# Performance work log

Measured on AMD Instinct MI355X. Metric: run time of the kernel, lower is better.

The kernel has to match this reference:

```python
import jax, jax.numpy as jnp
import numpy as np

B, T, I, H, A = 32, 1024, 64, 512, 16


def setup_inputs() -> dict:
    key = jax.random.key(0)
    ks = jax.random.split(key, 8)
    # xavier-normal-ish scales (faithful to init distribution family, values are arbitrary for a numeric baseline)
    def xavier(k, shape):
        fan_in, fan_out = shape[0], shape[1]
        std = (2.0 / (fan_in + fan_out)) ** 0.5
        return jax.random.normal(k, shape, dtype=jnp.float32) * std
    inp = jax.random.normal(ks[0], (B, T, I), dtype=jnp.float32)
    hn = jax.random.normal(ks[1], (1, B, H), dtype=jnp.float32)
    w_hh = xavier(ks[2], (H, H))          # weight_l0_hh: [hid, hid]
    w_ih = xavier(ks[3], (I, H))          # weight_l0_ih: [inp, hid]
    # torch Linear(hid, hid): y = x @ W.T + b; store already-transposed [in, out]
    fc1_w = xavier(ks[4], (H, H))
    fc1_b = jax.random.normal(ks[5], (H,), dtype=jnp.float32) * 0.01
    fc2_w = xavier(ks[6], (H, A))
    fc2_b = jax.random.normal(ks[7], (A,), dtype=jnp.float32) * 0.01
    return {"inp": inp, "hn": hn, "w_hh": w_hh, "w_ih": w_ih,
            "fc1_w": fc1_w, "fc1_b": fc1_b, "fc2_w": fc2_w, "fc2_b": fc2_b}


def reference(inp, hn, w_hh, w_ih, fc1_w, fc1_b, fc2_w, fc2_b):
    h0 = hn[0]                                  # [B, H]  (hn.squeeze(0))
    # precompute input projection for all steps: [T, B, H]
    x_proj = jnp.einsum('bti,ih->tbh', inp, w_ih)
    def step(h, xp_t):
        h_next = jax.nn.sigmoid(h @ w_hh + xp_t)  # [B, H]
        return h_next, h_next
    _, hs = jax.lax.scan(step, h0, x_proj)       # hs: [T, B, H]
    rnn_out = jnp.swapaxes(hs, 0, 1)             # [B, T, H]
    hn_last = rnn_out[:, -1, :][None]            # [1, B, H]
    hidden = jax.nn.relu(rnn_out @ fc1_w + fc1_b)
    out = jax.nn.sigmoid(hidden @ fc2_w + fc2_b) # [B, T, A]
    return (out, hn_last, rnn_out)
```

## Files before the change

### kernel.cpp

```cpp
#include <hip/hip_runtime.h>
#include <hip/hip_bf16.h>

#define Bz 32
#define Tz 1024
#define Iz 64
#define Hz 512
#define Az 16
#define NB 16

#define OFF_HN  (Bz*Tz*Az)
#define OFF_RNN (OFF_HN + Bz*Hz)

typedef unsigned short u16;
typedef unsigned int u32;
typedef unsigned long long u64;
typedef __attribute__((ext_vector_type(8))) unsigned short u16x8;
typedef __attribute__((ext_vector_type(8))) __bf16 bf16x8;
typedef __attribute__((ext_vector_type(4))) float f32x4;
typedef __attribute__((ext_vector_type(2))) float f32x2;

#define WS_FLAGS 0x00000u
#define WS_RING  0x21000u
#define WS_WHH   0x41000u
#define WS_WIH   0xC1000u
#define WS_W1T   0xD1000u
#define WS_ZERO  0x11000u

__device__ __forceinline__ u16 f2bf(float f) {
  union { float f; unsigned int i; } x; x.f = f;
  unsigned int r = (x.i + 0x7FFFu + ((x.i >> 16) & 1u)) >> 16;
  return (u16)r;
}
__device__ __forceinline__ float bf2f(u16 u) {
  union { unsigned int i; float f; } x; x.i = ((unsigned int)u) << 16; return x.f;
}
__device__ __forceinline__ float sigmoidf_(float z) {
  return 1.0f / (1.0f + __expf(-z));
}

__global__ void prep_kernel(const float* __restrict__ whh,
                            const float* __restrict__ wih,
                            const float* __restrict__ w1,
                            u16* __restrict__ whh_bf,
                            u16* __restrict__ wih_bf,
                            u16* __restrict__ w1t_bf) {
  int idx = blockIdx.x * 256 + threadIdx.x;
  if (idx < 262144) {
    whh_bf[idx] = f2bf(whh[idx]);
  } else if (idx < 294912) {
    int i = idx - 262144;
    wih_bf[i] = f2bf(wih[i]);
  } else if (idx < 557056) {
    int j = idx - 294912;
    int n = j >> 9, k = j & 511;
    w1t_bf[n * Hz + k] = f2bf(w1[k * Hz + n]);
  }
}

__global__ __launch_bounds__(512, 1) void rnn_scan_kernel(
    const float* __restrict__ inp,
    const float* __restrict__ hn,
    const u16* __restrict__ whh_bf,
    const u16* __restrict__ wih_bf,
    float* __restrict__ out_rnn,
    float* __restrict__ out_hn,
    int* __restrict__ flags,
    u16* __restrict__ hbuf)
{
  __shared__ float part[8 * 32 * 33];

  const int tid  = threadIdx.x;
  const int lane = tid & 63;
  const int w    = tid >> 6;
  const int ln   = lane & 15;
  const int q    = lane >> 4;
  const int c0   = blockIdx.x * 32;
  const int k0   = w * 64;

  bf16x8 bhh[2][2];
#pragma unroll
  for (int ct = 0; ct < 2; ++ct)
#pragma unroll
    for (int kc = 0; kc < 2; ++kc) {
      u16x8 f;
#pragma unroll
      for (int j = 0; j < 8; ++j)
        f[j] = whh_bf[(k0 + kc * 32 + q * 8 + j) * Hz + c0 + ct * 16 + ln];
      bhh[ct][kc] = __builtin_bit_cast(bf16x8, f);
    }

  bf16x8 bih[2];
  if (w < 2) {
#pragma unroll
    for (int ct = 0; ct < 2; ++ct) {
      u16x8 f;
#pragma unroll
      for (int j = 0; j < 8; ++j)
        f[j] = wih_bf[(w * 32 + q * 8 + j) * Hz + c0 + ct * 16 + ln];
      bih[ct] = __builtin_bit_cast(bf16x8, f);
    }
  }

  const int orow = tid >> 4;
  const int ocp  = tid & 15;
  const int ocol = c0 + ocp * 2;

  {
    u32 pk = (u32)f2bf(hn[orow * Hz + ocol]) |
             ((u32)f2bf(hn[orow * Hz + ocol + 1]) << 16);
    __hip_atomic_store((u32*)(hbuf + orow * Hz + ocol), pk, __ATOMIC_RELAXED,
                       __HIP_MEMORY_SCOPE_AGENT);
  }
  __syncthreads();
  if (tid == 0)
    __hip_atomic_store(&flags[blockIdx.x], 1, __ATOMIC_RELAXED,
                       __HIP_MEMORY_SCOPE_AGENT);

  for (int t = 0; t < Tz; ++t) {
    f32x4 xl0, xh0, xl1, xh1;
    if (w < 2) {
      const float* p0 = inp + ((size_t)(ln)      * Tz + t) * Iz + w * 32 + q * 8;
      const float* p1 = inp + ((size_t)(16 + ln) * Tz + t) * Iz + w * 32 + q * 8;
      xl0 = *(const f32x4*)p0; xh0 = *(const f32x4*)(p0 + 4);
      xl1 = *(const f32x4*)p1; xh1 = *(const f32x4*)(p1 + 4);
    }

    {
      const int sb = 2 * w + (lane & 1);
      int got;
      do {
        got = __hip_atomic_load(&flags[t * NB + sb], __ATOMIC_RELAXED,
                                __HIP_MEMORY_SCOPE_AGENT);
      } while (!__all(got));
    }

    const u64* hb = (const u64*)hbuf + (size_t)(t & 3) * (Bz * Hz / 4);
    u64 hr[8];
#pragma unroll
    for (int rt = 0; rt < 2; ++rt)
#pragma unroll
      for (int kc = 0; kc < 2; ++kc) {
        const u64* p = hb + (size_t)(rt * 16 + ln) * (Hz / 4) + w * 16 +
                       kc * 8 + q * 2;
        hr[rt * 4 + kc * 2 + 0] = __hip_atomic_load(
            p, __ATOMIC_RELAXED, __HIP_MEMORY_SCOPE_AGENT);
        hr[rt * 4 + kc * 2 + 1] = __hip_atomic_load(
            p + 1, __ATOMIC_RELAXED, __HIP_MEMORY_SCOPE_AGENT);
      }

    f32x4 acc[2][2];
#pragma unroll
    for (int rt = 0; rt < 2; ++rt)
#pragma unroll
      for (int ct = 0; ct < 2; ++ct) acc[rt][ct] = (f32x4){0.f, 0.f, 0.f, 0.f};

    if (w < 2) {
      u16x8 ax0, ax1;
#pragma unroll
      for (int j = 0; j < 4; ++j) {
        ax0[j]     = f2bf(xl0[j]);
        ax0[4 + j] = f2bf(xh0[j]);
        ax1[j]     = f2bf(xl1[j]);
        ax1[4 + j] = f2bf(xh1[j]);
      }
#pragma unroll
      for (int ct = 0; ct < 2; ++ct) {
        acc[0][ct] = __builtin_amdgcn_mfma_f32_16x16x32_bf16(
            __builtin_bit_cast(bf16x8, ax0), bih[ct], acc[0][ct], 0, 0, 0);
        acc[1][ct] = __builtin_amdgcn_mfma_f32_16x16x32_bf16(
            __builtin_bit_cast(bf16x8, ax1), bih[ct], acc[1][ct], 0, 0, 0);
      }
    }

#pragma unroll
    for (int kc = 0; kc < 2; ++kc)
#pragma unroll
      for (int rt = 0; rt < 2; ++rt) {
        u64 v[2] = {hr[rt * 4 + kc * 2], hr[rt * 4 + kc * 2 + 1]};
        bf16x8 af = __builtin_bit_cast(bf16x8, v);
#pragma unroll
        for (int ct = 0; ct < 2; ++ct)
          acc[rt][ct] = __builtin_amdgcn_mfma_f32_16x16x32_bf16(
              af, bhh[ct][kc], acc[rt][ct], 0, 0, 0);
      }

#pragma unroll
    for (int rt = 0; rt < 2; ++rt)
#pragma unroll
      for (int ct = 0; ct < 2; ++ct)
#pragma unroll
        for (int r = 0; r < 4; ++r)
          part[w * 1056 + (rt * 16 + q * 4 + r) * 33 + ct * 16 + ln] =
              acc[rt][ct][r];
    __syncthreads();

    float z0 = 0.f, z1 = 0.f;
#pragma unroll
    for (int ww = 0; ww < 8; ++ww) {
      z0 += part[ww * 1056 + orow * 33 + ocp * 2];
      z1 += part[ww * 1056 + orow * 33 + ocp * 2 + 1];
    }
    float h0 = sigmoidf_(z0), h1 = sigmoidf_(z1);
    u16* hbn = hbuf + ((t + 1) & 3) * (Bz * Hz);
    u32 pk = (u32)f2bf(h0) | ((u32)f2bf(h1) << 16);
    __hip_atomic_store((u32*)(hbn + orow * Hz + ocol), pk, __ATOMIC_RELAXED,
                       __HIP_MEMORY_SCOPE_AGENT);
    __syncthreads();
    if (tid == 0)
      __hip_atomic_store(&flags[(t + 1) * NB + blockIdx.x], 1, __ATOMIC_RELAXED,
                         __HIP_MEMORY_SCOPE_AGENT);

    f32x2 o2 = {h0, h1};
    *(f32x2*)(out_rnn + ((size_t)orow * Tz + t) * Hz + ocol) = o2;
    if (t == Tz - 1) *(f32x2*)(out_hn + orow * Hz + ocol) = o2;
  }
}

__global__ __launch_bounds__(256, 2) void fc_kernel(
    const float* __restrict__ X,
    const u16* __restrict__ w1t,
    const float* __restrict__ b1,
    const float* __restrict__ w2,
    const float* __restrict__ b2,
    float* __restrict__ out)
{
  __shared__ u16 smem[18432];
  u16* As = smem;
  u16* Bs = smem + 9216;
  u16* Ht = smem;

  const int tid  = threadIdx.x;
  const int lane = tid & 63;
  const int wv   = tid >> 6;
  const int ln   = lane & 15, q = lane >> 4;
  const int mq   = (wv & 1) * 64, nq = (wv >> 1) * 64;
  const size_t r0 = (size_t)blockIdx.x * 128;
  const int om = tid >> 1;
  const int oa = (tid & 1) * 8;

  float oacc[8];
#pragma unroll
  for (int j = 0; j < 8; ++j) oacc[j] = 0.f;

  for (int nt = 0; nt < 4; ++nt) {
    const int n0 = nt * 128;
    f32x4 acc[4][4];
#pragma unroll
    for (int mi = 0; mi < 4; ++mi)
#pragma unroll
      for (int ni = 0; ni < 4; ++ni) acc[mi][ni] = (f32x4){0.f, 0.f, 0.f, 0.f};

    for (int kb = 0; kb < 8; ++kb) {
      const int K0 = kb * 64;
      __syncthreads();
      for (int i = tid; i < 1024; i += 256) {
        int row = i >> 3, c = (i & 7) * 8;
        f32x4 lo = *(const f32x4*)(X + (r0 + row) * Hz + K0 + c);
        f32x4 hi = *(const f32x4*)(X + (r0 + row) * Hz + K0 + c + 4);
        u16x8 p;
#pragma unroll
        for (int j = 0; j < 4; ++j) { p[j] = f2bf(lo[j]); p[4 + j] = f2bf(hi[j]); }
        *(u16x8*)(As + row * 72 + c) = p;
      }
      for (int i = tid; i < 1024; i += 256) {
        int row = i >> 3, c = (i & 7) * 8;
        *(u16x8*)(Bs + row * 72 + c) =
            *(const u16x8*)(w1t + (size_t)(n0 + row) * Hz + K0 + c);
      }
      __syncthreads();
#pragma unroll
      for (int kt = 0; kt < 2; ++kt) {
        bf16x8 af[4], bfr[4];
#pragma unroll
        for (int mi = 0; mi < 4; ++mi)
          af[mi] = __builtin_bit_cast(
              bf16x8,
              *(const u16x8*)(As + (mq + mi * 16 + ln) * 72 + kt * 32 + q * 8));
#pragma unroll
        for (int ni = 0; ni < 4; ++ni)
          bfr[ni] = __builtin_bit_cast(
              bf16x8,
              *(const u16x8*)(Bs + (nq + ni * 16 + ln) * 72 + kt * 32 + q * 8));
#pragma unroll
        for (int mi = 0; mi < 4; ++mi)
#pragma unroll
          for (int ni = 0; ni < 4; ++ni)
            acc[mi][ni] = __builtin_amdgcn_mfma_f32_16x16x32_bf16(
                af[mi], bfr[ni], acc[mi][ni], 0, 0, 0);
      }
    }
    __syncthreads();

#pragma unroll
    for (int ni = 0; ni < 4; ++ni) {
      float bb = b1[n0 + nq + ni * 16 + ln];
#pragma unroll
      for (int mi = 0; mi < 4; ++mi)
#pragma unroll
        for (int r = 0; r < 4; ++r) {
          float h = fmaxf(acc[mi][ni][r] + bb, 0.f);
          Ht[(mq + mi * 16 + q * 4 + r) * 136 + nq + ni * 16 + ln] = f2bf(h);
        }
    }
    __syncthreads();

    for (int n = 0; n < 128; ++n) {
      float hv = bf2f(Ht[om * 136 + n]);
      const float* w2p = w2 + (size_t)(n0 + n) * Az + oa;
#pragma unroll
      for (int j = 0; j < 8; ++j) oacc[j] += hv * w2p[j];
    }
  }

#pragma unroll
  for (int j = 0; j < 8; ++j)
    out[(r0 + om) * Az + oa + j] = sigmoidf_(oacc[j] + b2[oa + j]);
}

extern "C" void kernel_launch(void* const* d_in, const int* in_sizes, int n_in,
                              void* d_out, int out_size, void* d_ws, size_t ws_size,
                              hipStream_t stream) {
  int idx_inp = 0, idx_hn = 1, idx_wih = 3, idx_b1 = 5, idx_w2 = 6, idx_b2 = 7;
  int amb1 = -1, amb2 = -1, found = 0;
  for (int i = 0; i < 8 && i < n_in; ++i) {
    switch (in_sizes[i]) {
      case 2097152: idx_inp = i; found |= 1; break;
      case 16384:   idx_hn  = i; found |= 2; break;
      case 32768:   idx_wih = i; found |= 4; break;
      case 512:     idx_b1  = i; found |= 8; break;
      case 8192:    idx_w2  = i; found |= 16; break;
      case 16:      idx_b2  = i; found |= 32; break;
      case 262144:  if (amb1 < 0) amb1 = i; else amb2 = i; break;
    }
  }
  int idx_whh = 2, idx_w1 = 4;
  if (amb1 >= 0 && amb2 >= 0 && found == 63) {
    if (idx_b1 < idx_inp) { idx_w1 = amb1; idx_whh = amb2; }
    else                  { idx_whh = amb1; idx_w1 = amb2; }
  }

  const float* inp = (const float*)d_in[idx_inp];
  const float* hn  = (const float*)d_in[idx_hn];
  const float* whh = (const float*)d_in[idx_whh];
  const float* wih = (const float*)d_in[idx_wih];
  const float* w1  = (const float*)d_in[idx_w1];
  const float* b1  = (const float*)d_in[idx_b1];
  const float* w2  = (const float*)d_in[idx_w2];
  const float* b2  = (const float*)d_in[idx_b2];

  float* out     = (float*)d_out;
  float* out_hn  = out + OFF_HN;
  float* out_rnn = out + OFF_RNN;

  char* ws    = (char*)d_ws;
  int* flags  = (int*)(ws + WS_FLAGS);
  u16* hbuf   = (u16*)(ws + WS_RING);
  u16* whh_bf = (u16*)(ws + WS_WHH);
  u16* wih_bf = (u16*)(ws + WS_WIH);
  u16* w1t_bf = (u16*)(ws + WS_W1T);

  (void)hipMemsetAsync(d_ws, 0, WS_ZERO, stream);
  prep_kernel<<<dim3(2176), dim3(256), 0, stream>>>(whh, wih, w1,
                                                    whh_bf, wih_bf, w1t_bf);
  rnn_scan_kernel<<<dim3(NB), dim3(512), 0, stream>>>(
      inp, hn, whh_bf, wih_bf, out_rnn, out_hn, flags, hbuf);
  fc_kernel<<<dim3(256), dim3(256), 0, stream>>>(
      out_rnn, w1t_bf, b1, w2, b2, out);
}
```

Baseline: 3.408 ms.

## Repartition RNN scan into paired blocks with local-half overlap and partner-only sync

The recurrent scan moves from 16 blocks, each owning 32 columns for all batch rows and syncing with all others, to 4 blocks organised as pairs. Each pair owns 16 batch rows and each block owns half the hidden columns, holding its full K-slice of W_hh in registers. Each block computes its local-half contribution from an LDS copy of its own previous outputs before waiting on a single partner flag, then reads only the partner's half from global memory. This removes the cross-wave LDS reduction and most of the all-to-all flag polling. In exchange it uses many more registers for the weight fragments and runs on far fewer CUs.

```diff
diff --git a/kernel.cpp b/kernel.cpp
--- a/kernel.cpp
+++ b/kernel.cpp
@@ -6,7 +6,7 @@
 #define Iz 64
 #define Hz 512
 #define Az 16
-#define NB 16
+#define NBLK 4
 
 #define OFF_HN  (Bz*Tz*Az)
 #define OFF_RNN (OFF_HN + Bz*Hz)
@@ -17,7 +17,6 @@
 typedef __attribute__((ext_vector_type(8))) unsigned short u16x8;
 typedef __attribute__((ext_vector_type(8))) __bf16 bf16x8;
 typedef __attribute__((ext_vector_type(4))) float f32x4;
-typedef __attribute__((ext_vector_type(2))) float f32x2;
 
 #define WS_FLAGS 0x00000u
 #define WS_RING  0x21000u
@@ -57,7 +56,7 @@
   }
 }
 
-__global__ __launch_bounds__(512, 1) void rnn_scan_kernel(
+__global__ __launch_bounds__(512, 2) void rnn_scan_kernel(
     const float* __restrict__ inp,
     const float* __restrict__ hn,
     const u16* __restrict__ whh_bf,
@@ -67,17 +66,36 @@
     int* __restrict__ flags,
     u16* __restrict__ hbuf)
 {
-  __shared__ float part[8 * 32 * 33];
+  __shared__ u16 hlds[2][16][264];
 
   const int tid  = threadIdx.x;
   const int lane = tid & 63;
   const int w    = tid >> 6;
   const int ln   = lane & 15;
   const int q    = lane >> 4;
-  const int c0   = blockIdx.x * 32;
-  const int k0   = w * 64;
-
-  bf16x8 bhh[2][2];
+  const int bid  = blockIdx.x;
+  const int qh   = bid & 1;
+  const int p    = bid >> 1;
+  const int r0   = p * 16;
+  const int cbase = qh * 256;
+  const int obase = (1 - qh) * 256;
+  const int c0   = cbase + w * 32;
+  const int partner = bid ^ 1;
+
+  bf16x8 bhh[2][16];
+#pragma unroll
+  for (int ct = 0; ct < 2; ++ct)
+#pragma unroll
+    for (int ks = 0; ks < 16; ++ks) {
+      const int kg = (ks < 8) ? (cbase + ks * 32) : (obase + (ks - 8) * 32);
+      u16x8 f;
+#pragma unroll
+      for (int j = 0; j < 8; ++j)
+        f[j] = whh_bf[(kg + q * 8 + j) * Hz + c0 + ct * 16 + ln];
+      bhh[ct][ks] = __builtin_bit_cast(bf16x8, f);
+    }
+
+  bf16x8 bih[2][2];
 #pragma unroll
   for (int ct = 0; ct < 2; ++ct)
 #pragma unroll
@@ -85,134 +103,134 @@
       u16x8 f;
 #pragma unroll
       for (int j = 0; j < 8; ++j)
-        f[j] = whh_bf[(k0 + kc * 32 + q * 8 + j) * Hz + c0 + ct * 16 + ln];
-      bhh[ct][kc] = __builtin_bit_cast(bf16x8, f);
-    }
-
-  bf16x8 bih[2];
-  if (w < 2) {
-#pragma unroll
-    for (int ct = 0; ct < 2; ++ct) {
-      u16x8 f;
-#pragma unroll
-      for (int j = 0; j < 8; ++j)
-        f[j] = wih_bf[(w * 32 + q * 8 + j) * Hz + c0 + ct * 16 + ln];
-      bih[ct] = __builtin_bit_cast(bf16x8, f);
-    }
-  }
-
-  const int orow = tid >> 4;
-  const int ocp  = tid & 15;
-  const int ocol = c0 + ocp * 2;
+        f[j] = wih_bf[(kc * 32 + q * 8 + j) * Hz + c0 + ct * 16 + ln];
+      bih[ct][kc] = __builtin_bit_cast(bf16x8, f);
+    }
 
   {
-    u32 pk = (u32)f2bf(hn[orow * Hz + ocol]) |
-             ((u32)f2bf(hn[orow * Hz + ocol + 1]) << 16);
-    __hip_atomic_store((u32*)(hbuf + orow * Hz + ocol), pk, __ATOMIC_RELAXED,
-                       __HIP_MEMORY_SCOPE_AGENT);
+    const int lrow = tid >> 5;
+    const int cc   = (tid & 31) * 8;
+    f32x4 a = *(const f32x4*)(hn + (size_t)(r0 + lrow) * Hz + cbase + cc);
+    f32x4 b = *(const f32x4*)(hn + (size_t)(r0 + lrow) * Hz + cbase + cc + 4);
+    u16x8 px;
+#pragma unroll
+    for (int j = 0; j < 4; ++j) { px[j] = f2bf(a[j]); px[4 + j] = f2bf(b[j]); }
+    *(u16x8*)&hlds[0][lrow][cc] = px;
+    u32* rp = (u32*)(hbuf + (size_t)(r0 + lrow) * Hz + cbase + cc);
+#pragma unroll
+    for (int k = 0; k < 4; ++k) {
+      u32 pk = (u32)px[2 * k] | ((u32)px[2 * k + 1] << 16);
+      __hip_atomic_store(rp + k, pk, __ATOMIC_RELAXED, __HIP_MEMORY_SCOPE_AGENT);
+    }
   }
   __syncthreads();
   if (tid == 0)
-    __hip_atomic_store(&flags[blockIdx.x], 1, __ATOMIC_RELAXED,
+    __hip_atomic_store(&flags[bid], 1, __ATOMIC_RELAXED,
                        __HIP_MEMORY_SCOPE_AGENT);
 
   for (int t = 0; t < Tz; ++t) {
-    f32x4 xl0, xh0, xl1, xh1;
-    if (w < 2) {
-      const float* p0 = inp + ((size_t)(ln)      * Tz + t) * Iz + w * 32 + q * 8;
-      const float* p1 = inp + ((size_t)(16 + ln) * Tz + t) * Iz + w * 32 + q * 8;
-      xl0 = *(const f32x4*)p0; xh0 = *(const f32x4*)(p0 + 4);
-      xl1 = *(const f32x4*)p1; xh1 = *(const f32x4*)(p1 + 4);
+    const int cur = t & 1;
+
+    const float* ip = inp + ((size_t)(r0 + ln) * Tz + t) * Iz + q * 8;
+    f32x4 x0 = *(const f32x4*)(ip);
+    f32x4 x1 = *(const f32x4*)(ip + 4);
+    f32x4 x2 = *(const f32x4*)(ip + 32);
+    f32x4 x3 = *(const f32x4*)(ip + 36);
+    u16x8 ax0, ax1;
+#pragma unroll
+    for (int j = 0; j < 4; ++j) {
+      ax0[j]     = f2bf(x0[j]);
+      ax0[4 + j] = f2bf(x1[j]);
+      ax1[j]     = f2bf(x2[j]);
+      ax1[4 + j] = f2bf(x3[j]);
+    }
+
+    f32x4 acc[2];
+    acc[0] = (f32x4){0.f, 0.f, 0.f, 0.f};
+    acc[1] = (f32x4){0.f, 0.f, 0.f, 0.f};
+
+#pragma unroll
+    for (int ct = 0; ct < 2; ++ct) {
+      acc[ct] = __builtin_amdgcn_mfma_f32_16x16x32_bf16(
+          __builtin_bit_cast(bf16x8, ax0), bih[ct][0], acc[ct], 0, 0, 0);
+      acc[ct] = __builtin_amdgcn_mfma_f32_16x16x32_bf16(
+          __builtin_bit_cast(bf16x8, ax1), bih[ct][1], acc[ct], 0, 0, 0);
+    }
+
+#pragma unroll
+    for (int ks = 0; ks < 8; ++ks) {
+      bf16x8 afr = __builtin_bit_cast(
+          bf16x8, *(const u16x8*)&hlds[cur][ln][ks * 32 + q * 8]);
+#pragma unroll
+      for (int ct = 0; ct < 2; ++ct)
+        acc[ct] = __builtin_amdgcn_mfma_f32_16x16x32_bf16(
+            afr, bhh[ct][ks], acc[ct], 0, 0, 0);
     }
 
     {
-      const int sb = 2 * w + (lane & 1);
       int got;
       do {
-        got = __hip_atomic_load(&flags[t * NB + sb], __ATOMIC_RELAXED,
+        got = __hip_atomic_load(&flags[t * NBLK + partner], __ATOMIC_RELAXED,
                                 __HIP_MEMORY_SCOPE_AGENT);
-      } while (!__all(got));
-    }
-
-    const u64* hb = (const u64*)hbuf + (size_t)(t & 3) * (Bz * Hz / 4);
-    u64 hr[8];
-#pragma unroll
-    for (int rt = 0; rt < 2; ++rt)
-#pragma unroll
-      for (int kc = 0; kc < 2; ++kc) {
-        const u64* p = hb + (size_t)(rt * 16 + ln) * (Hz / 4) + w * 16 +
-                       kc * 8 + q * 2;
-        hr[rt * 4 + kc * 2 + 0] = __hip_atomic_load(
-            p, __ATOMIC_RELAXED, __HIP_MEMORY_SCOPE_AGENT);
-        hr[rt * 4 + kc * 2 + 1] = __hip_atomic_load(
-            p + 1, __ATOMIC_RELAXED, __HIP_MEMORY_SCOPE_AGENT);
-      }
-
-    f32x4 acc[2][2];
-#pragma unroll
-    for (int rt = 0; rt < 2; ++rt)
-#pragma unroll
-      for (int ct = 0; ct < 2; ++ct) acc[rt][ct] = (f32x4){0.f, 0.f, 0.f, 0.f};
-
-    if (w < 2) {
-      u16x8 ax0, ax1;
-#pragma unroll
-      for (int j = 0; j < 4; ++j) {
-        ax0[j]     = f2bf(xl0[j]);
-        ax0[4 + j] = f2bf(xh0[j]);
-        ax1[j]     = f2bf(xl1[j]);
-        ax1[4 + j] = f2bf(xh1[j]);
-      }
-#pragma unroll
-      for (int ct = 0; ct < 2; ++ct) {
-        acc[0][ct] = __builtin_amdgcn_mfma_f32_16x16x32_bf16(
-            __builtin_bit_cast(bf16x8, ax0), bih[ct], acc[0][ct], 0, 0, 0);
-        acc[1][ct] = __builtin_amdgcn_mfma_f32_16x16x32_bf16(
-            __builtin_bit_cast(bf16x8, ax1), bih[ct], acc[1][ct], 0, 0, 0);
-      }
-    }
-
-#pragma unroll
-    for (int kc = 0; kc < 2; ++kc)
-#pragma unroll
-      for (int rt = 0; rt < 2; ++rt) {
-        u64 v[2] = {hr[rt * 4 + kc * 2], hr[rt * 4 + kc * 2 + 1]};
-        bf16x8 af = __builtin_bit_cast(bf16x8, v);
-#pragma unroll
-        for (int ct = 0; ct < 2; ++ct)
-          acc[rt][ct] = __builtin_amdgcn_mfma_f32_16x16x32_bf16(
-              af, bhh[ct][kc], acc[rt][ct], 0, 0, 0);
-      }
-
-#pragma unroll
-    for (int rt = 0; rt < 2; ++rt)
+      } while (!got);
+    }
+
+    const u64* pb = (const u64*)hbuf + (size_t)(t & 3) * (Bz * Hz / 4) +
+                    (size_t)(r0 + ln) * (Hz / 4) + (obase / 4);
+    u64 hr[16];
+#pragma unroll
+    for (int ks2 = 0; ks2 < 8; ++ks2) {
+      hr[2 * ks2]     = __hip_atomic_load(pb + ks2 * 8 + q * 2,
+                                          __ATOMIC_RELAXED,
+                                          __HIP_MEMORY_SCOPE_AGENT);
+      hr[2 * ks2 + 1] = __hip_atomic_load(pb + ks2 * 8 + q * 2 + 1,
+                                          __ATOMIC_RELAXED,
+                                          __HIP_MEMORY_SCOPE_AGENT);
+    }
+#pragma unroll
+    for (int ks2 = 0; ks2 < 8; ++ks2) {
+      u64 v[2] = {hr[2 * ks2], hr[2 * ks2 + 1]};
+      bf16x8 afr = __builtin_bit_cast(bf16x8, v);
 #pragma unroll
       for (int ct = 0; ct < 2; ++ct)
-#pragma unroll
-        for (int r = 0; r < 4; ++r)
-          part[w * 1056 + (rt * 16 + q * 4 + r) * 33 + ct * 16 + ln] =
-              acc[rt][ct][r];
-    __syncthreads();
-
-    float z0 = 0.f, z1 = 0.f;
-#pragma unroll
-    for (int ww = 0; ww < 8; ++ww) {
-      z0 += part[ww * 1056 + orow * 33 + ocp * 2];
-      z1 += part[ww * 1056 + orow * 33 + ocp * 2 + 1];
-    }
-    float h0 = sigmoidf_(z0), h1 = sigmoidf_(z1);
-    u16* hbn = hbuf + ((t + 1) & 3) * (Bz * Hz);
-    u32 pk = (u32)f2bf(h0) | ((u32)f2bf(h1) << 16);
-    __hip_atomic_store((u32*)(hbn + orow * Hz + ocol), pk, __ATOMIC_RELAXED,
-                       __HIP_MEMORY_SCOPE_AGENT);
+        acc[ct] = __builtin_amdgcn_mfma_f32_16x16x32_bf16(
+            afr, bhh[ct][8 + ks2], acc[ct], 0, 0, 0);
+    }
+
+    const int nxt = cur ^ 1;
+    u16* ring_next = hbuf + (size_t)((t + 1) & 3) * (Bz * Hz);
+    float hv[2][4];
+#pragma unroll
+    for (int ct = 0; ct < 2; ++ct)
+#pragma unroll
+      for (int r = 0; r < 4; ++r) {
+        hv[ct][r] = sigmoidf_(acc[ct][r]);
+        u32 mine  = (u32)f2bf(hv[ct][r]);
+        u32 other = (u32)__shfl_xor((int)mine, 1, 64);
+        if (!(ln & 1)) {
+          u32 pk = mine | (other << 16);
+          const int lrow = q * 4 + r;
+          const int lcol = w * 32 + ct * 16 + ln;
+          __hip_atomic_store(
+              (u32*)(ring_next + (size_t)(r0 + lrow) * Hz + cbase + lcol), pk,
+              __ATOMIC_RELAXED, __HIP_MEMORY_SCOPE_AGENT);
+          *(u32*)&hlds[nxt][lrow][lcol] = pk;
+        }
+      }
     __syncthreads();
     if (tid == 0)
-      __hip_atomic_store(&flags[(t + 1) * NB + blockIdx.x], 1, __ATOMIC_RELAXED,
+      __hip_atomic_store(&flags[(t + 1) * NBLK + bid], 1, __ATOMIC_RELAXED,
                          __HIP_MEMORY_SCOPE_AGENT);
 
-    f32x2 o2 = {h0, h1};
-    *(f32x2*)(out_rnn + ((size_t)orow * Tz + t) * Hz + ocol) = o2;
-    if (t == Tz - 1) *(f32x2*)(out_hn + orow * Hz + ocol) = o2;
+#pragma unroll
+    for (int ct = 0; ct < 2; ++ct)
+#pragma unroll
+      for (int r = 0; r < 4; ++r) {
+        const int grow = r0 + q * 4 + r;
+        const int gcol = c0 + ct * 16 + ln;
+        out_rnn[((size_t)grow * Tz + t) * Hz + gcol] = hv[ct][r];
+        if (t == Tz - 1) out_hn[(size_t)grow * Hz + gcol] = hv[ct][r];
+      }
   }
 }
 
@@ -257,10 +275,10 @@
         int row = i >> 3, c = (i & 7) * 8;
         f32x4 lo = *(const f32x4*)(X + (r0 + row) * Hz + K0 + c);
         f32x4 hi = *(const f32x4*)(X + (r0 + row) * Hz + K0 + c + 4);
-        u16x8 p;
-#pragma unroll
-        for (int j = 0; j < 4; ++j) { p[j] = f2bf(lo[j]); p[4 + j] = f2bf(hi[j]); }
-        *(u16x8*)(As + row * 72 + c) = p;
+        u16x8 pxx;
+#pragma unroll
+        for (int j = 0; j < 4; ++j) { pxx[j] = f2bf(lo[j]); pxx[4 + j] = f2bf(hi[j]); }
+        *(u16x8*)(As + row * 72 + c) = pxx;
       }
       for (int i = tid; i < 1024; i += 256) {
         int row = i >> 3, c = (i & 7) * 8;
@@ -362,7 +380,7 @@
   (void)hipMemsetAsync(d_ws, 0, WS_ZERO, stream);
   prep_kernel<<<dim3(2176), dim3(256), 0, stream>>>(whh, wih, w1,
                                                     whh_bf, wih_bf, w1t_bf);
-  rnn_scan_kernel<<<dim3(NB), dim3(512), 0, stream>>>(
+  rnn_scan_kernel<<<dim3(NBLK), dim3(512), 0, stream>>>(
       inp, hn, whh_bf, wih_bf, out_rnn, out_hn, flags, hbuf);
   fc_kernel<<<dim3(256), dim3(256), 0, stream>>>(
       out_rnn, w1t_bf, b1, w2, b2, out);
```

Measured after the change: 6.797 ms. 99.4% more time.
